# Kernel optimization log

Measured on AMD Instinct MI355X. Metric: run time of the kernel, lower is better.

Reference implementation:

```python
import jax, jax.numpy as jnp
import numpy as np

B, C, D, H, W = 4096, 64, 4, 4, 4
E, DIM = 16384, 4096  # num_embeddings, embedding_dim = C*D*H*W
COMMITMENT_COST = 0.25


def setup_inputs() -> dict:
    key = jax.random.key(0)
    k1, k2 = jax.random.split(key)
    inputs = jax.random.normal(k1, (B, C, D, H, W), dtype=jnp.float32)
    limit = 1.0 / E
    embed_w = jax.random.uniform(k2, (E, DIM), dtype=jnp.float32,
                                 minval=-limit, maxval=limit)
    return {"inputs": inputs, "embed_w": embed_w}


def reference(inputs, embed_w):
    sg = jax.lax.stop_gradient
    input_shape = inputs.shape
    flat = inputs.reshape(inputs.shape[0], -1)  # [B, DIM]
    distances = (jnp.sum(flat * flat, axis=1, keepdims=True)
                 + jnp.sum(embed_w * embed_w, axis=1)
                 - 2.0 * jnp.matmul(flat, embed_w.T))
    encoding_indices = jnp.argmin(distances, axis=1)  # [B]
    encodings = jax.nn.one_hot(encoding_indices, E, dtype=jnp.float32)  # [B, E]
    # gather nearest codebook vectors (same math as one_hot @ embed_w)
    quantized = embed_w[encoding_indices].reshape(input_shape)
    e_latent_loss = jnp.mean((sg(quantized) - inputs) ** 2)
    q_latent_loss = jnp.mean((quantized - sg(inputs)) ** 2)
    loss = q_latent_loss + COMMITMENT_COST * e_latent_loss
    # straight-through estimator
    quantized = inputs + sg(quantized - inputs)
    avg_probs = jnp.mean(encodings, axis=0)  # [E]
    perplexity = jnp.exp(-jnp.sum(avg_probs * jnp.log(avg_probs + 1e-10)))
    return loss, quantized, perplexity, encodings
```

## Files before the change

### kernel.cpp

```cpp
#include <hip/hip_runtime.h>

typedef unsigned long long u64;
typedef unsigned int u32;
typedef unsigned short u16;

typedef __attribute__((ext_vector_type(8))) short short8;
typedef __attribute__((ext_vector_type(4))) short short4v;
typedef __attribute__((ext_vector_type(4))) float floatx4;
typedef __attribute__((ext_vector_type(4))) int int4v;

static constexpr int BROWS = 4096;
static constexpr int ENUM_ = 16384;
static constexpr int KD    = 4096;
static constexpr int CANDMAX = 65536;
#define MARGIN 6e-4f


__device__ __forceinline__ u32 sortable(float d) {
  u32 u = __float_as_uint(d);
  return (u & 0x80000000u) ? ~u : (u | 0x80000000u);
}
__device__ __forceinline__ float unsortable(u32 k) {
  u32 u = (k & 0x80000000u) ? (k & 0x7fffffffu) : ~k;
  return __uint_as_float(u);
}

__device__ __forceinline__ u16 f2bf_rn(float f) {
  u32 u = __float_as_uint(f);
  u32 r = (u + 0x7fffu + ((u >> 16) & 1u)) >> 16;
  return (u16)r;
}
__device__ __forceinline__ float bf2f(u16 h) {
  return __uint_as_float((u32)h << 16);
}

__device__ __forceinline__ void gload_lds16(const void* g, void* l) {
  __builtin_amdgcn_global_load_lds((const __attribute__((address_space(1))) void*)g,
                                   (__attribute__((address_space(3))) void*)l,
                                   16, 0, 0);
}

__device__ __forceinline__ float blockReduceSumF(float v) {
  __shared__ float s[4];
  #pragma unroll
  for (int o = 32; o > 0; o >>= 1) v += __shfl_down(v, o);
  int lane = threadIdx.x & 63, wid = threadIdx.x >> 6;
  if (lane == 0) s[wid] = v;
  __syncthreads();
  float r = 0.f;
  if (threadIdx.x == 0) r = s[0] + s[1] + s[2] + s[3];
  return r;
}

__device__ __forceinline__ double blockReduceSumD(double v) {
  __shared__ double s[4];
  #pragma unroll
  for (int o = 32; o > 0; o >>= 1) v += __shfl_down(v, o);
  int lane = threadIdx.x & 63, wid = threadIdx.x >> 6;
  if (lane == 0) s[wid] = v;
  __syncthreads();
  double r = 0.0;
  if (threadIdx.x == 0) r = s[0] + s[1] + s[2] + s[3];
  return r;
}


__global__ __launch_bounds__(256) void quant_x(const float* __restrict__ x,
                                               signed char* __restrict__ xq,
                                               float* __restrict__ sx) {
  int i = blockIdx.x;
  const float4* xr = (const float4*)(x + (size_t)i * KD);
  float4 v[4];
  float mx = 0.f;
  #pragma unroll
  for (int t = 0; t < 4; ++t) {
    v[t] = xr[threadIdx.x + t * 256];
    mx = fmaxf(mx, fmaxf(fmaxf(fabsf(v[t].x), fabsf(v[t].y)),
                         fmaxf(fabsf(v[t].z), fabsf(v[t].w))));
  }
  #pragma unroll
  for (int o = 32; o > 0; o >>= 1) mx = fmaxf(mx, __shfl_down(mx, o));
  __shared__ float red[4];
  int lane = threadIdx.x & 63, wid = threadIdx.x >> 6;
  if (lane == 0) red[wid] = mx;
  __syncthreads();
  float m = fmaxf(fmaxf(red[0], red[1]), fmaxf(red[2], red[3]));
  float inv = m > 0.f ? 127.f / m : 0.f;
  u32* qr = (u32*)(xq + (size_t)i * KD);
  #pragma unroll
  for (int t = 0; t < 4; ++t) {
    int e = threadIdx.x + t * 256;
    int q0 = __float2int_rn(v[t].x * inv);
    int q1 = __float2int_rn(v[t].y * inv);
    int q2 = __float2int_rn(v[t].z * inv);
    int q3 = __float2int_rn(v[t].w * inv);
    qr[e] = ((u32)(q0 & 0xff)) | ((u32)(q1 & 0xff) << 8) |
            ((u32)(q2 & 0xff) << 16) | ((u32)(q3 & 0xff) << 24);
  }
  if (threadIdx.x == 0) sx[i] = m * (1.f / 127.f);
}

__global__ __launch_bounds__(256) void quant_w_e2(const float* __restrict__ w,
                                                  signed char* __restrict__ wq,
                                                  float* __restrict__ sw,
                                                  float* __restrict__ e2) {
  int j = blockIdx.x;
  const float4* wr = (const float4*)(w + (size_t)j * KD);
  float4 v[4];
  float mx = 0.f, s2 = 0.f;
  #pragma unroll
  for (int t = 0; t < 4; ++t) {
    v[t] = wr[threadIdx.x + t * 256];
    s2 += v[t].x * v[t].x + v[t].y * v[t].y + v[t].z * v[t].z + v[t].w * v[t].w;
    mx = fmaxf(mx, fmaxf(fmaxf(fabsf(v[t].x), fabsf(v[t].y)),
                         fmaxf(fabsf(v[t].z), fabsf(v[t].w))));
  }
  #pragma unroll
  for (int o = 32; o > 0; o >>= 1) {
    s2 += __shfl_down(s2, o);
    mx = fmaxf(mx, __shfl_down(mx, o));
  }
  __shared__ float redS[4], redM[4];
  int lane = threadIdx.x & 63, wid = threadIdx.x >> 6;
  if (lane == 0) { redS[wid] = s2; redM[wid] = mx; }
  __syncthreads();
  float m = fmaxf(fmaxf(redM[0], redM[1]), fmaxf(redM[2], redM[3]));
  float inv = m > 0.f ? 127.f / m : 0.f;
  u32* qr = (u32*)(wq + (size_t)j * KD);
  #pragma unroll
  for (int t = 0; t < 4; ++t) {
    int e = threadIdx.x + t * 256;
    int q0 = __float2int_rn(v[t].x * inv);
    int q1 = __float2int_rn(v[t].y * inv);
    int q2 = __float2int_rn(v[t].z * inv);
    int q3 = __float2int_rn(v[t].w * inv);
    qr[e] = ((u32)(q0 & 0xff)) | ((u32)(q1 & 0xff) << 8) |
            ((u32)(q2 & 0xff) << 16) | ((u32)(q3 & 0xff) << 24);
  }
  if (threadIdx.x == 0) {
    sw[j] = m * (1.f / 127.f);
    e2[j] = redS[0] + redS[1] + redS[2] + redS[3];
  }
}

__global__ __launch_bounds__(256) void split_kernel(const float* __restrict__ src,
                                                    u16* __restrict__ hi,
                                                    u16* __restrict__ lo, int n8) {
  int t = blockIdx.x * 256 + threadIdx.x;
  if (t >= n8) return;
  const float4* s = (const float4*)src + (size_t)t * 2;
  float4 a = s[0], b = s[1];
  float v[8] = {a.x, a.y, a.z, a.w, b.x, b.y, b.z, b.w};
  short h[8], l[8];
  #pragma unroll
  for (int i = 0; i < 8; ++i) {
    u16 hh = f2bf_rn(v[i]);
    h[i] = (short)hh;
    l[i] = (short)f2bf_rn(v[i] - bf2f(hh));
  }
  *(short8*)(hi + (size_t)t * 8) = *(short8*)h;
  *(short8*)(lo + (size_t)t * 8) = *(short8*)l;
}

__global__ __launch_bounds__(256) void e2_kernel(const float* __restrict__ w,
                                                 float* __restrict__ e2) {
  int j = blockIdx.x;
  const float4* wr = (const float4*)(w + (size_t)j * KD);
  float local = 0.f;
  #pragma unroll
  for (int t = 0; t < 4; ++t) {
    float4 v = wr[threadIdx.x + t * 256];
    local += v.x * v.x + v.y * v.y + v.z * v.z + v.w * v.w;
  }
  float tot = blockReduceSumF(local);
  if (threadIdx.x == 0) e2[j] = tot;
}

__global__ __launch_bounds__(512, 2)
void gemm_i8(const signed char* __restrict__ Aq, const signed char* __restrict__ Bq,
             const float* __restrict__ sx, const float* __restrict__ sw,
             const float* __restrict__ e2, u16* __restrict__ dist,
             u64* __restrict__ best) {
  __shared__ char smem[131072];
  constexpr int NT = KD / 128;

  const u32 wg = blockIdx.x;
  const u32 swz = (wg & 7) * 128 + (wg >> 3);
  const int by = swz & 15;
  const int bx = swz >> 4;
  const int row0 = by * 256, col0 = bx * 256;

  const int t = threadIdx.x;
  const int lane = t & 63, wv = t >> 6;
  const int wr = wv >> 2, wc = wv & 3;
  const int quad = lane >> 4, lcol = lane & 15;

  const int m0 = t >> 2;
  const int g0 = (t & 3) ^ ((t >> 3) & 3);
  const size_t aG0 = (size_t)(row0 + m0) * KD + g0 * 16;
  const size_t bG0 = (size_t)(col0 + m0) * KD + g0 * 16;
  const size_t rowStep = (size_t)128 * KD;

  auto stage = [&](int tau, int k) {
    if (tau >= NT) return;
    char* base = smem + (tau & 1) * 65536 +
                 (k == 0 ? 0 : (k == 1 ? 32768 : (k == 2 ? 16384 : 49152)));
    size_t gofs = ((k == 0 || k == 2) ? aG0 : bG0) +
                  (size_t)tau * 128 + (k >= 2 ? 64 : 0);
    const signed char* src = (k == 0 || k == 2) ? Aq : Bq;
    gload_lds16(src + gofs, base + t * 16);
    gload_lds16(src + gofs + rowStep, base + t * 16 + 8192);
  };

  stage(0, 0); stage(0, 1); stage(0, 2); stage(0, 3);
  stage(1, 0); stage(1, 1);
  asm volatile("s_waitcnt vmcnt(4)" ::: "memory");
  asm volatile("s_barrier" ::: "memory");

  int4v acc[8][4] = {};

  for (int tt = 0; tt < NT; ++tt) {
    char* buf = smem + (tt & 1) * 65536;
    int4v bf[4];
    #pragma unroll
    for (int c = 0; c < 4; ++c) {
      const int ks = c >> 1, mh = c & 1;
      const char* Ar = buf + ks * 16384;
      const char* Br = buf + 32768 + ks * 16384;

      int4v af[4];
      #pragma unroll
      for (int r = 0; r < 4; ++r) {
        int m = wr * 128 + mh * 64 + r * 16 + lcol;
        af[r] = *(const int4v*)(Ar + m * 64 + ((quad ^ ((m >> 1) & 3)) << 4));
      }
      if (mh == 0) {
        #pragma unroll
        for (int n = 0; n < 4; ++n) {
          int mm = wc * 64 + n * 16 + lcol;
          bf[n] = *(const int4v*)(Br + mm * 64 + ((quad ^ ((mm >> 1) & 3)) << 4));
        }
      }

      if (c == 0)      stage(tt + 1, 2);
      else if (c == 1) stage(tt + 1, 3);
      else if (c == 2) stage(tt + 2, 0);
      else             stage(tt + 2, 1);

      asm volatile("s_barrier" ::: "memory");
      __builtin_amdgcn_s_setprio(1);
      #pragma unroll
      for (int r = 0; r < 4; ++r)
        #pragma unroll
        for (int n = 0; n < 4; ++n)
          acc[mh * 4 + r][n] = __builtin_amdgcn_mfma_i32_16x16x64_i8(
              af[r], bf[n], acc[mh * 4 + r][n], 0, 0, 0);
      __builtin_amdgcn_s_setprio(0);
      if (c == 3) asm volatile("s_waitcnt vmcnt(4)" ::: "memory");
      asm volatile("s_barrier" ::: "memory");
    }
  }

  float e2v[4], sc2[4];
  #pragma unroll
  for (int n = 0; n < 4; ++n) {
    int gc = col0 + wc * 64 + n * 16 + lcol;
    e2v[n] = e2[gc];
    sc2[n] = -2.0f * sw[gc];
  }

  #pragma unroll
  for (int fm = 0; fm < 8; ++fm) {
    #pragma unroll
    for (int i = 0; i < 4; ++i) {
      int grow = row0 + wr * 128 + fm * 16 + quad * 4 + i;
      float sxr = sx[grow];
      u64 kmin = ~0ull;
      #pragma unroll
      for (int n = 0; n < 4; ++n) {
        int gcol = col0 + wc * 64 + n * 16 + lcol;
        float d = __fadd_rn(e2v[n],
                            __fmul_rn(sc2[n] * sxr, (float)acc[fm][n][i]));
        dist[(size_t)grow * ENUM_ + gcol] = f2bf_rn(d);
        u64 key = ((u64)sortable(d) << 32) | (u32)gcol;
        kmin = key < kmin ? key : kmin;
      }
      #pragma unroll
      for (int msk = 1; msk < 16; msk <<= 1) {
        u64 o = __shfl_xor(kmin, msk);
        kmin = o < kmin ? o : kmin;
      }
      if (lcol == 0) atomicMin(&best[grow], kmin);
    }
  }
}

__global__ __launch_bounds__(256)
void scan_kernel(const u16* __restrict__ dist, const u64* __restrict__ best,
                 u64* __restrict__ cand, int* __restrict__ ccount) {
  const int n8 = BROWS * ENUM_ / 8;
  int step = gridDim.x * 256;
  for (int f = blockIdx.x * 256 + threadIdx.x; f < n8; f += step) {
    int i = f >> 11;
    float limit = unsortable((u32)(best[i] >> 32)) + MARGIN;
    short8 v = ((const short8*)dist)[f];
    #pragma unroll
    for (int e = 0; e < 8; ++e) {
      float d = bf2f((u16)v[e]);
      if (d <= limit) {
        int pos = atomicAdd(ccount, 1);
        if (pos < CANDMAX) cand[pos] = ((u64)(u32)i << 32) | (u32)(f * 8 + e - i * ENUM_);
      }
    }
  }
}

__global__ __launch_bounds__(256)
void refine_kernel(const float* __restrict__ x, const float* __restrict__ w,
                   const u64* __restrict__ cand, const int* __restrict__ ccount,
                   u64* __restrict__ best2) {
  int cnt = *ccount;
  if (cnt > CANDMAX) cnt = CANDMAX;
  for (int b = blockIdx.x; b < cnt; b += gridDim.x) {
    u64 cd = cand[b];
    int i = (int)(cd >> 32), j = (int)(cd & 0xffffffffu);
    const float4* xr = (const float4*)(x + (size_t)i * KD);
    const float4* wr = (const float4*)(w + (size_t)j * KD);
    double local = 0.0;
    #pragma unroll
    for (int t = 0; t < 4; ++t) {
      int e = threadIdx.x + t * 256;
      float4 xv = xr[e], wv = wr[e];
      local += (double)wv.x * ((double)wv.x - 2.0 * (double)xv.x)
             + (double)wv.y * ((double)wv.y - 2.0 * (double)xv.y)
             + (double)wv.z * ((double)wv.z - 2.0 * (double)xv.z)
             + (double)wv.w * ((double)wv.w - 2.0 * (double)xv.w);
    }
    double d = blockReduceSumD(local);
    if (threadIdx.x == 0) {
      u64 key = ((u64)sortable((float)d) << 32) | (u32)j;
      atomicMin(&best2[i], key);
    }
    __syncthreads();
  }
}

__global__ __launch_bounds__(256)
void gemm_argmin_mfma(const u16* __restrict__ Ah, const u16* __restrict__ Al,
                      const u16* __restrict__ Bh, const u16* __restrict__ Bl,
                      const float* __restrict__ e2, u64* __restrict__ best) {
  __shared__ char smem[32768];
  const int by = blockIdx.x, bx = blockIdx.y;
  const int row0 = by * 128, col0 = bx * 128;
  const int t = threadIdx.x;
  const int lane = t & 63, wv = t >> 6;
  const int wr = wv >> 1, wc = wv & 1;
  const int srow = t >> 2;
  const int schunk = (t & 3) ^ ((t >> 3) & 3);
  const size_t aoff0 = (size_t)(row0 + srow) * KD + schunk * 8;
  const size_t aoff1 = aoff0 + (size_t)64 * KD;
  const size_t boff0 = (size_t)(col0 + srow) * KD + schunk * 8;
  const size_t boff1 = boff0 + (size_t)64 * KD;
  char* sAh = smem; char* sAl = smem + 8192;
  char* sBh = smem + 16384; char* sBl = smem + 24576;
  const int d0 = t * 16, d1 = 4096 + t * 16;
  floatx4 acc[4][4] = {};
  for (int kk = 0; kk < KD; kk += 32) {
    __syncthreads();
    gload_lds16(Ah + aoff0 + kk, sAh + d0);
    gload_lds16(Ah + aoff1 + kk, sAh + d1);
    gload_lds16(Al + aoff0 + kk, sAl + d0);
    gload_lds16(Al + aoff1 + kk, sAl + d1);
    gload_lds16(Bh + boff0 + kk, sBh + d0);
    gload_lds16(Bh + boff1 + kk, sBh + d1);
    gload_lds16(Bl + boff0 + kk, sBl + d0);
    gload_lds16(Bl + boff1 + kk, sBl + d1);
    __syncthreads();
    short8 afh[4], afl[4];
    #pragma unroll
    for (int r = 0; r < 4; ++r) {
      int m = wr * 64 + r * 16 + (lane & 15);
      int off = m * 64 + (((lane >> 4) ^ ((m >> 1) & 3)) * 16);
      afh[r] = *(const short8*)(sAh + off);
      afl[r] = *(const short8*)(sAl + off);
    }
    #pragma unroll
    for (int c = 0; c < 4; ++c) {
      int m = wc * 64 + c * 16 + (lane & 15);
      int off = m * 64 + (((lane >> 4) ^ ((m >> 1) & 3)) * 16);
      short8 bfh = *(const short8*)(sBh + off);
      short8 bfl = *(const short8*)(sBl + off);
      #pragma unroll
      for (int r = 0; r < 4; ++r) {
        acc[r][c] = __builtin_amdgcn_mfma_f32_16x16x32_bf16(afh[r], bfh, acc[r][c], 0, 0, 0);
        acc[r][c] = __builtin_amdgcn_mfma_f32_16x16x32_bf16(afl[r], bfh, acc[r][c], 0, 0, 0);
        acc[r][c] = __builtin_amdgcn_mfma_f32_16x16x32_bf16(afh[r], bfl, acc[r][c], 0, 0, 0);
      }
    }
  }
  const int quad = lane >> 4, lcol = lane & 15;
  float e2v[4];
  #pragma unroll
  for (int c = 0; c < 4; ++c) e2v[c] = e2[col0 + wc * 64 + c * 16 + lcol];
  #pragma unroll
  for (int r = 0; r < 4; ++r) {
    #pragma unroll
    for (int i = 0; i < 4; ++i) {
      int grow = row0 + wr * 64 + r * 16 + quad * 4 + i;
      u64 kmin = ~0ull;
      #pragma unroll
      for (int c = 0; c < 4; ++c) {
        int gcol = col0 + wc * 64 + c * 16 + lcol;
        float d = __fadd_rn(e2v[c], __fmul_rn(-2.0f, acc[r][c][i]));
        u64 key = ((u64)sortable(d) << 32) | (u32)gcol;
        kmin = key < kmin ? key : kmin;
      }
      #pragma unroll
      for (int msk = 1; msk < 16; msk <<= 1) {
        u64 o = __shfl_xor(kmin, msk);
        kmin = o < kmin ? o : kmin;
      }
      if (lcol == 0) atomicMin(&best[grow], kmin);
    }
  }
}

__global__ __launch_bounds__(256)
void gemm_argmin(const float* __restrict__ A, const float* __restrict__ W,
                 const float* __restrict__ e2, u64* __restrict__ best) {
  __shared__ union {
    struct { float As[8][128]; float Bs[8][128]; } st;
    u64 red[128 * 16];
  } sm;
  const int by = blockIdx.x, bx = blockIdx.y;
  const int tid = threadIdx.x;
  const int tx = tid & 15, ty = tid >> 4;
  const int row0 = by * 128, col0 = bx * 128;
  const int lm = tid >> 1, lk = (tid & 1) * 4;
  const float* Ap = A + (size_t)(row0 + lm) * KD + lk;
  const float* Wp = W + (size_t)(col0 + lm) * KD + lk;
  float acc[8][8];
  #pragma unroll
  for (int r = 0; r < 8; ++r)
    #pragma unroll
    for (int c = 0; c < 8; ++c) acc[r][c] = 0.f;
  for (int kk = 0; kk < KD; kk += 8) {
    float4 av = *(const float4*)(Ap + kk);
    float4 bv = *(const float4*)(Wp + kk);
    __syncthreads();
    sm.st.As[lk + 0][lm] = av.x; sm.st.As[lk + 1][lm] = av.y;
    sm.st.As[lk + 2][lm] = av.z; sm.st.As[lk + 3][lm] = av.w;
    sm.st.Bs[lk + 0][lm] = bv.x; sm.st.Bs[lk + 1][lm] = bv.y;
    sm.st.Bs[lk + 2][lm] = bv.z; sm.st.Bs[lk + 3][lm] = bv.w;
    __syncthreads();
    #pragma unroll
    for (int k = 0; k < 8; ++k) {
      float a[8], b[8];
      *(float4*)&a[0] = *(const float4*)&sm.st.As[k][ty * 8];
      *(float4*)&a[4] = *(const float4*)&sm.st.As[k][ty * 8 + 4];
      *(float4*)&b[0] = *(const float4*)&sm.st.Bs[k][tx * 8];
      *(float4*)&b[4] = *(const float4*)&sm.st.Bs[k][tx * 8 + 4];
      #pragma unroll
      for (int r = 0; r < 8; ++r)
        #pragma unroll
        for (int c = 0; c < 8; ++c)
          acc[r][c] = fmaf(a[r], b[c], acc[r][c]);
    }
  }
  __syncthreads();
  float e2v[8];
  #pragma unroll
  for (int c = 0; c < 8; ++c) e2v[c] = e2[col0 + tx * 8 + c];
  #pragma unroll
  for (int r = 0; r < 8; ++r) {
    u64 bk = ~0ull;
    #pragma unroll
    for (int c = 0; c < 8; ++c) {
      int col = col0 + tx * 8 + c;
      float d = fmaf(-2.0f, acc[r][c], e2v[c]);
      u64 key = ((u64)sortable(d) << 32) | (u32)col;
      bk = key < bk ? key : bk;
    }
    sm.red[(ty * 8 + r) * 16 + tx] = bk;
  }
  __syncthreads();
  if (tid < 128) {
    u64 m = sm.red[tid * 16];
    #pragma unroll
    for (int t2 = 1; t2 < 16; ++t2) {
      u64 v = sm.red[tid * 16 + t2];
      m = v < m ? v : m;
    }
    atomicMin(&best[row0 + tid], m);
  }
}


__global__ __launch_bounds__(256) void scatter_kernel(const u64* __restrict__ best,
                                                      int* __restrict__ idx,
                                                      int* __restrict__ counts,
                                                      float* __restrict__ enc) {
  int i = blockIdx.x * 256 + threadIdx.x;
  u64 k = best[i];
  int j = (int)(k & 0xffffffffu);
  idx[i] = j;
  atomicAdd(&counts[j], 1);
  enc[(size_t)i * ENUM_ + j] = 1.0f;
}

__global__ __launch_bounds__(256) void gather_loss(const float* __restrict__ x,
                                                   const float* __restrict__ w,
                                                   const int* __restrict__ idx,
                                                   float* __restrict__ quant,
                                                   double* __restrict__ accum) {
  int i = blockIdx.x;
  int j = idx[i];
  const float4* wr = (const float4*)(w + (size_t)j * KD);
  const float4* xr = (const float4*)(x + (size_t)i * KD);
  float* qr = quant + (size_t)i * KD;
  double local = 0.0;
  #pragma unroll
  for (int t = 0; t < 4; ++t) {
    int e = threadIdx.x + t * 256;
    float4 wv = wr[e];
    float4 xv = xr[e];
    qr[4 * e + 0] = wv.x; qr[4 * e + 1] = wv.y;
    qr[4 * e + 2] = wv.z; qr[4 * e + 3] = wv.w;
    double d0 = (double)wv.x - (double)xv.x;
    double d1 = (double)wv.y - (double)xv.y;
    double d2 = (double)wv.z - (double)xv.z;
    double d3 = (double)wv.w - (double)xv.w;
    local += d0 * d0 + d1 * d1 + d2 * d2 + d3 * d3;
  }
  double tot = blockReduceSumD(local);
  if (threadIdx.x == 0) atomicAdd(accum, tot);
}

__global__ __launch_bounds__(256) void scalars_kernel(const int* __restrict__ counts,
                                                      const double* __restrict__ accum,
                                                      float* __restrict__ loss_out,
                                                      float* __restrict__ perp_out) {
  double local = 0.0;
  for (int j = threadIdx.x; j < ENUM_; j += 256) {
    double p = (double)counts[j] * (1.0 / 4096.0);
    local += p * log(p + 1e-10);
  }
  double s = blockReduceSumD(local);
  if (threadIdx.x == 0) {
    double mean = (*accum) * (1.0 / ((double)BROWS * (double)KD));
    loss_out[0] = (float)(1.25 * mean);
    perp_out[0] = (float)exp(-s);
  }
}


extern "C" void kernel_launch(void* const* d_in, const int* in_sizes, int n_in,
                              void* d_out, int out_size, void* d_ws, size_t ws_size,
                              hipStream_t stream) {
  const float* x = (const float*)d_in[0];
  const float* w = (const float*)d_in[1];
  float* out = (float*)d_out;

  char* ws = (char*)d_ws;
  u64* best     = (u64*)ws;
  u64* best2    = (u64*)(ws + 32768);
  int* idx      = (int*)(ws + 65536);
  int* counts   = (int*)(ws + 81920);
  double* accum = (double*)(ws + 147456);
  int* ccount   = (int*)(ws + 147464);
  float* e2     = (float*)(ws + 163840);
  u64* cand     = (u64*)(ws + 229376);

  signed char* x_q = (signed char*)(ws + 753664);
  signed char* w_q = (signed char*)(ws + 17530880);
  float* s_x    = (float*)(ws + 84639744);
  float* s_w    = (float*)(ws + 84656128);
  u16* dist     = (u16*)(ws + 84721664);
  const size_t NEED_FR = 84721664ull + 134217728ull;

  u16* x_hi     = (u16*)(ws + 753664);
  u16* w_hi     = (u16*)(ws + 753664 + 33554432ull);
  char* regionO = ws + 753664 + 33554432ull + 134217728ull;
  u16* x_lo     = (u16*)regionO;
  u16* w_lo     = (u16*)(regionO + 33554432ull);
  const size_t NEED_3T = 168525824ull + 167772160ull;

  float* loss_out = out;
  float* quant    = out + 1;
  float* perp_out = out + 16777217;
  float* enc      = out + 16777218;

  hipMemsetAsync(best, 0xFF, 65536, stream);
  hipMemsetAsync(counts, 0, 65536 + 16, stream);
  hipMemsetAsync(enc, 0, (size_t)BROWS * ENUM_ * sizeof(float), stream);

  if (ws_size >= NEED_FR) {
    quant_x<<<BROWS, 256, 0, stream>>>(x, x_q, s_x);
    quant_w_e2<<<ENUM_, 256, 0, stream>>>(w, w_q, s_w, e2);
    gemm_i8<<<1024, 512, 0, stream>>>(x_q, w_q, s_x, s_w, e2, dist, best);
    scan_kernel<<<4096, 256, 0, stream>>>(dist, best, cand, ccount);
    refine_kernel<<<4096, 256, 0, stream>>>(x, w, cand, ccount, best2);
    scatter_kernel<<<BROWS / 256, 256, 0, stream>>>(best2, idx, counts, enc);
  } else if (ws_size >= NEED_3T) {
    e2_kernel<<<ENUM_, 256, 0, stream>>>(w, e2);
    split_kernel<<<BROWS * KD / 8 / 256, 256, 0, stream>>>(x, x_hi, x_lo, BROWS * KD / 8);
    split_kernel<<<ENUM_ * KD / 8 / 256, 256, 0, stream>>>(w, w_hi, w_lo, ENUM_ * KD / 8);
    gemm_argmin_mfma<<<dim3(32, 128), 256, 0, stream>>>(x_hi, x_lo, w_hi, w_lo, e2, best);
    scatter_kernel<<<BROWS / 256, 256, 0, stream>>>(best, idx, counts, enc);
  } else {
    e2_kernel<<<ENUM_, 256, 0, stream>>>(w, e2);
    gemm_argmin<<<dim3(32, 128), 256, 0, stream>>>(x, w, e2, best);
    scatter_kernel<<<BROWS / 256, 256, 0, stream>>>(best, idx, counts, enc);
  }
  gather_loss<<<BROWS, 256, 0, stream>>>(x, w, idx, quant, accum);
  scalars_kernel<<<1, 256, 0, stream>>>(counts, accum, loss_out, perp_out);
}
```

Baseline: 1.065 ms.

## Restage int8 GEMM LDS tiles, fuse one-hot fill, vectorize quant stores

The int8 GEMM now stages 128-byte K rows per tile with an 8-way XOR swizzle, and loads all B fragments once per tile. The four sub-steps per tile become two compute phases, with A/B prefetch spread across them. The separate 256MB memset of the one-hot output is replaced by a per-row kernel that writes zeros and the single one in one pass, saving a full extra write of that buffer. The quantized output stores are vectorized, and the perplexity log uses a fast float intrinsic, which may cost some precision.

Result: faster. 1.044 ms (-2.0%).

```diff
diff --git a/kernel.cpp b/kernel.cpp
--- a/kernel.cpp
+++ b/kernel.cpp
@@ -8,6 +8,7 @@
 typedef __attribute__((ext_vector_type(4))) short short4v;
 typedef __attribute__((ext_vector_type(4))) float floatx4;
 typedef __attribute__((ext_vector_type(4))) int int4v;
+typedef float float4a __attribute__((ext_vector_type(4), aligned(4)));
 
 static constexpr int BROWS = 4096;
 static constexpr int ENUM_ = 16384;
@@ -195,70 +196,89 @@
   const int wr = wv >> 2, wc = wv & 3;
   const int quad = lane >> 4, lcol = lane & 15;
 
-  const int m0 = t >> 2;
-  const int g0 = (t & 3) ^ ((t >> 3) & 3);
-  const size_t aG0 = (size_t)(row0 + m0) * KD + g0 * 16;
-  const size_t bG0 = (size_t)(col0 + m0) * KD + g0 * 16;
-  const size_t rowStep = (size_t)128 * KD;
-
-  auto stage = [&](int tau, int k) {
+  const int srow = t >> 3;
+  const int g0 = (t & 7) ^ ((t >> 3) & 7);
+  const size_t aBase = (size_t)(row0 + srow) * KD + g0 * 16;
+  const size_t bBase = (size_t)(col0 + srow) * KD + g0 * 16;
+
+  auto stageA = [&](int tau, int q) {
     if (tau >= NT) return;
-    char* base = smem + (tau & 1) * 65536 +
-                 (k == 0 ? 0 : (k == 1 ? 32768 : (k == 2 ? 16384 : 49152)));
-    size_t gofs = ((k == 0 || k == 2) ? aG0 : bG0) +
-                  (size_t)tau * 128 + (k >= 2 ? 64 : 0);
-    const signed char* src = (k == 0 || k == 2) ? Aq : Bq;
-    gload_lds16(src + gofs, base + t * 16);
-    gload_lds16(src + gofs + rowStep, base + t * 16 + 8192);
+    gload_lds16(Aq + aBase + (size_t)(q * 64) * KD + (size_t)tau * 128,
+                smem + (tau & 1) * 65536 + q * 8192 + t * 16);
   };
-
-  stage(0, 0); stage(0, 1); stage(0, 2); stage(0, 3);
-  stage(1, 0); stage(1, 1);
-  asm volatile("s_waitcnt vmcnt(4)" ::: "memory");
+  auto stageB = [&](int tau, int q) {
+    if (tau >= NT) return;
+    gload_lds16(Bq + bBase + (size_t)(q * 64) * KD + (size_t)tau * 128,
+                smem + (tau & 1) * 65536 + 32768 + q * 8192 + t * 16);
+  };
+
+  stageA(0, 0); stageA(0, 1); stageA(0, 2); stageA(0, 3);
+  stageB(0, 0); stageB(0, 1); stageB(0, 2); stageB(0, 3);
+  stageA(1, 0); stageA(1, 2);
+  stageB(1, 0); stageB(1, 1); stageB(1, 2); stageB(1, 3);
+  asm volatile("s_waitcnt vmcnt(6)" ::: "memory");
   asm volatile("s_barrier" ::: "memory");
 
   int4v acc[8][4] = {};
 
   for (int tt = 0; tt < NT; ++tt) {
-    char* buf = smem + (tt & 1) * 65536;
-    int4v bf[4];
-    #pragma unroll
-    for (int c = 0; c < 4; ++c) {
-      const int ks = c >> 1, mh = c & 1;
-      const char* Ar = buf + ks * 16384;
-      const char* Br = buf + 32768 + ks * 16384;
-
-      int4v af[4];
-      #pragma unroll
-      for (int r = 0; r < 4; ++r) {
-        int m = wr * 128 + mh * 64 + r * 16 + lcol;
-        af[r] = *(const int4v*)(Ar + m * 64 + ((quad ^ ((m >> 1) & 3)) << 4));
-      }
-      if (mh == 0) {
-        #pragma unroll
-        for (int n = 0; n < 4; ++n) {
-          int mm = wc * 64 + n * 16 + lcol;
-          bf[n] = *(const int4v*)(Br + mm * 64 + ((quad ^ ((mm >> 1) & 3)) << 4));
-        }
-      }
-
-      if (c == 0)      stage(tt + 1, 2);
-      else if (c == 1) stage(tt + 1, 3);
-      else if (c == 2) stage(tt + 2, 0);
-      else             stage(tt + 2, 1);
-
-      asm volatile("s_barrier" ::: "memory");
-      __builtin_amdgcn_s_setprio(1);
+    const char* Ar = smem + (tt & 1) * 65536;
+    const char* Br = Ar + 32768;
+    int4v af[4][2], bf[4][2];
+
+    #pragma unroll
+    for (int r = 0; r < 4; ++r) {
+      int m = wr * 128 + r * 16 + lcol;
+      #pragma unroll
+      for (int k = 0; k < 2; ++k)
+        af[r][k] = *(const int4v*)(Ar + m * 128 + ((((k << 2) | quad) ^ (m & 7)) << 4));
+    }
+    #pragma unroll
+    for (int n = 0; n < 4; ++n) {
+      int mm = wc * 64 + n * 16 + lcol;
+      #pragma unroll
+      for (int k = 0; k < 2; ++k)
+        bf[n][k] = *(const int4v*)(Br + mm * 128 + ((((k << 2) | quad) ^ (mm & 7)) << 4));
+    }
+    stageA(tt + 1, 1); stageA(tt + 1, 3);
+    asm volatile("s_barrier" ::: "memory");
+    __builtin_amdgcn_s_setprio(1);
+    #pragma unroll
+    for (int k = 0; k < 2; ++k)
       #pragma unroll
       for (int r = 0; r < 4; ++r)
         #pragma unroll
         for (int n = 0; n < 4; ++n)
-          acc[mh * 4 + r][n] = __builtin_amdgcn_mfma_i32_16x16x64_i8(
-              af[r], bf[n], acc[mh * 4 + r][n], 0, 0, 0);
-      __builtin_amdgcn_s_setprio(0);
-      if (c == 3) asm volatile("s_waitcnt vmcnt(4)" ::: "memory");
-      asm volatile("s_barrier" ::: "memory");
-    }
+          acc[r][n] = __builtin_amdgcn_mfma_i32_16x16x64_i8(
+              af[r][k], bf[n][k], acc[r][n], 0, 0, 0);
+    __builtin_amdgcn_s_setprio(0);
+    asm volatile("s_barrier" ::: "memory");
+
+    #pragma unroll
+    for (int r = 0; r < 4; ++r) {
+      int m = wr * 128 + 64 + r * 16 + lcol;
+      #pragma unroll
+      for (int k = 0; k < 2; ++k)
+        af[r][k] = *(const int4v*)(Ar + m * 128 + ((((k << 2) | quad) ^ (m & 7)) << 4));
+    }
+    if (tt < NT - 2) {
+      stageA(tt + 2, 0); stageA(tt + 2, 2);
+      stageB(tt + 2, 0); stageB(tt + 2, 1); stageB(tt + 2, 2); stageB(tt + 2, 3);
+    }
+    asm volatile("s_barrier" ::: "memory");
+    __builtin_amdgcn_s_setprio(1);
+    #pragma unroll
+    for (int k = 0; k < 2; ++k)
+      #pragma unroll
+      for (int r = 0; r < 4; ++r)
+        #pragma unroll
+        for (int n = 0; n < 4; ++n)
+          acc[4 + r][n] = __builtin_amdgcn_mfma_i32_16x16x64_i8(
+              af[r][k], bf[n][k], acc[4 + r][n], 0, 0, 0);
+    __builtin_amdgcn_s_setprio(0);
+    if (tt < NT - 2) asm volatile("s_waitcnt vmcnt(6)" ::: "memory");
+    else             asm volatile("s_waitcnt vmcnt(0)" ::: "memory");
+    asm volatile("s_barrier" ::: "memory");
   }
 
   float e2v[4], sc2[4];
@@ -496,16 +516,26 @@
 }
 
 
-__global__ __launch_bounds__(256) void scatter_kernel(const u64* __restrict__ best,
-                                                      int* __restrict__ idx,
-                                                      int* __restrict__ counts,
-                                                      float* __restrict__ enc) {
-  int i = blockIdx.x * 256 + threadIdx.x;
+__global__ __launch_bounds__(256) void enc_fill(const u64* __restrict__ best,
+                                                int* __restrict__ idx,
+                                                int* __restrict__ counts,
+                                                float* __restrict__ enc) {
+  int i = blockIdx.x;
   u64 k = best[i];
   int j = (int)(k & 0xffffffffu);
-  idx[i] = j;
-  atomicAdd(&counts[j], 1);
-  enc[(size_t)i * ENUM_ + j] = 1.0f;
+  if (threadIdx.x == 0) {
+    idx[i] = j;
+    atomicAdd(&counts[j], 1);
+  }
+  float* er = enc + (size_t)i * ENUM_;
+  #pragma unroll
+  for (int tq = 0; tq < 16; ++tq) {
+    int e = threadIdx.x + tq * 256;
+    float4a z = {0.f, 0.f, 0.f, 0.f};
+    int base = e * 4;
+    if ((j >> 2) == e) z[j & 3] = 1.0f;
+    *(float4a*)(er + base) = z;
+  }
 }
 
 __global__ __launch_bounds__(256) void gather_loss(const float* __restrict__ x,
@@ -524,8 +554,8 @@
     int e = threadIdx.x + t * 256;
     float4 wv = wr[e];
     float4 xv = xr[e];
-    qr[4 * e + 0] = wv.x; qr[4 * e + 1] = wv.y;
-    qr[4 * e + 2] = wv.z; qr[4 * e + 3] = wv.w;
+    float4a q; q[0] = wv.x; q[1] = wv.y; q[2] = wv.z; q[3] = wv.w;
+    *(float4a*)(qr + 4 * e) = q;
     double d0 = (double)wv.x - (double)xv.x;
     double d1 = (double)wv.y - (double)xv.y;
     double d2 = (double)wv.z - (double)xv.z;
@@ -543,7 +573,7 @@
   double local = 0.0;
   for (int j = threadIdx.x; j < ENUM_; j += 256) {
     double p = (double)counts[j] * (1.0 / 4096.0);
-    local += p * log(p + 1e-10);
+    local += p * (double)__logf((float)(p + 1e-10));
   }
   double s = blockReduceSumD(local);
   if (threadIdx.x == 0) {
@@ -592,7 +622,6 @@
 
   hipMemsetAsync(best, 0xFF, 65536, stream);
   hipMemsetAsync(counts, 0, 65536 + 16, stream);
-  hipMemsetAsync(enc, 0, (size_t)BROWS * ENUM_ * sizeof(float), stream);
 
   if (ws_size >= NEED_FR) {
     quant_x<<<BROWS, 256, 0, stream>>>(x, x_q, s_x);
@@ -600,17 +629,17 @@
     gemm_i8<<<1024, 512, 0, stream>>>(x_q, w_q, s_x, s_w, e2, dist, best);
     scan_kernel<<<4096, 256, 0, stream>>>(dist, best, cand, ccount);
     refine_kernel<<<4096, 256, 0, stream>>>(x, w, cand, ccount, best2);
-    scatter_kernel<<<BROWS / 256, 256, 0, stream>>>(best2, idx, counts, enc);
+    enc_fill<<<BROWS, 256, 0, stream>>>(best2, idx, counts, enc);
   } else if (ws_size >= NEED_3T) {
     e2_kernel<<<ENUM_, 256, 0, stream>>>(w, e2);
     split_kernel<<<BROWS * KD / 8 / 256, 256, 0, stream>>>(x, x_hi, x_lo, BROWS * KD / 8);
     split_kernel<<<ENUM_ * KD / 8 / 256, 256, 0, stream>>>(w, w_hi, w_lo, ENUM_ * KD / 8);
     gemm_argmin_mfma<<<dim3(32, 128), 256, 0, stream>>>(x_hi, x_lo, w_hi, w_lo, e2, best);
-    scatter_kernel<<<BROWS / 256, 256, 0, stream>>>(best, idx, counts, enc);
+    enc_fill<<<BROWS, 256, 0, stream>>>(best, idx, counts, enc);
   } else {
     e2_kernel<<<ENUM_, 256, 0, stream>>>(w, e2);
     gemm_argmin<<<dim3(32, 128), 256, 0, stream>>>(x, w, e2, best);
-    scatter_kernel<<<BROWS / 256, 256, 0, stream>>>(best, idx, counts, enc);
+    enc_fill<<<BROWS, 256, 0, stream>>>(best, idx, counts, enc);
   }
   gather_loss<<<BROWS, 256, 0, stream>>>(x, w, idx, quant, accum);
   scalars_kernel<<<1, 256, 0, stream>>>(counts, accum, loss_out, perp_out);
```
